# Kernel optimization log

Measured on AMD Instinct MI355X. Metric: run time of the kernel, lower is better.

Reference implementation:

```python
import jax, jax.numpy as jnp
import numpy as np

NUM_LEVELS = 6
LEVEL_DIM = 4
BASE_RES = 4
HASHMAP_SIZE = 2 ** 19  # torch-ngp default log2_hashmap_size=19
N_SAMPLES = 300
PRIMES = (1, 2654435761, 805459861)
N_RAYS = 16384

# offsets of the 8 trilinear corners, [8,3]
_OFFS = jnp.array([[i, j, k] for i in (0, 1) for j in (0, 1) for k in (0, 1)], dtype=jnp.int32)


def _sample_points_along_ray(starts, ends):
    # starts/ends: [N,2]; lerp 300 points, append ray parameter t as z -> [N,300,3]
    t = jnp.linspace(0.0, 1.0, N_SAMPLES, dtype=starts.dtype)[None, :, None]  # [1,300,1]
    p2 = starts[:, None, :] * (1.0 - t) + ends[:, None, :] * t  # [N,300,2]
    z = jnp.broadcast_to(t, (starts.shape[0], N_SAMPLES, 1))
    return jnp.concatenate([p2, z], axis=-1)


def _grid_encode(points, embeddings):
    # points: [N,S,3] in [0,1]; embeddings: [L, T, D]. Returns [N,S,L*D].
    feats = []
    for l in range(NUM_LEVELS):
        R = BASE_RES * (2 ** l)  # 4,8,16,32,64,128
        pos = points * R
        p0 = jnp.floor(pos).astype(jnp.int32)
        w = pos - p0  # trilinear fractions, [N,S,3]
        corners = jnp.clip(p0[..., None, :] + _OFFS, 0, R)  # [N,S,8,3]
        cw = jnp.where(_OFFS.astype(bool), w[..., None, :], 1.0 - w[..., None, :]).prod(-1)  # [N,S,8]
        if (R + 1) ** 3 <= HASHMAP_SIZE:
            # dense level: row-major vertex index
            idx = corners[..., 0] + corners[..., 1] * (R + 1) + corners[..., 2] * (R + 1) ** 2
        else:
            # hashed level: xor of coord * prime, uint32 wraparound
            c = corners.astype(jnp.uint32)
            idx = ((c[..., 0] * jnp.uint32(PRIMES[0]))
                   ^ (c[..., 1] * jnp.uint32(PRIMES[1]))
                   ^ (c[..., 2] * jnp.uint32(PRIMES[2]))) % jnp.uint32(HASHMAP_SIZE)
            idx = idx.astype(jnp.int32)
        emb = embeddings[l][idx]  # [N,S,8,D] gather
        feats.append((cw[..., None] * emb).sum(-2))  # [N,S,D]
    return jnp.concatenate(feats, axis=-1)  # [N,S,24]


def setup_inputs() -> dict:
    key = jax.random.key(0)
    ks = jax.random.split(key, 12)
    x = jax.random.uniform(ks[0], (N_RAYS, 4), dtype=jnp.float32)
    indices_first = jax.random.randint(ks[1], (N_RAYS,), 0, N_SAMPLES, dtype=jnp.int32)
    # hash-grid tables, torch-ngp init: uniform(-1e-4, 1e-4)
    embeddings = jax.random.uniform(ks[2], (NUM_LEVELS, HASHMAP_SIZE, LEVEL_DIM),
                                    minval=-1e-4, maxval=1e-4, dtype=jnp.float32)
    d_in = NUM_LEVELS * LEVEL_DIM * 5  # 120
    sc = 0.02
    W1 = jax.random.normal(ks[3], (64, d_in), dtype=jnp.float32) * sc
    b1 = jnp.zeros((64,), jnp.float32)
    W2 = jax.random.normal(ks[4], (64, 64), dtype=jnp.float32) * sc
    b2 = jnp.zeros((64,), jnp.float32)
    W3 = jax.random.normal(ks[5], (64, 64), dtype=jnp.float32) * sc
    b3 = jnp.zeros((64,), jnp.float32)
    W4 = jax.random.normal(ks[6], (3, 64), dtype=jnp.float32) * sc
    b4 = jnp.zeros((3,), jnp.float32)
    return {"x": x, "indices_first": indices_first, "embeddings": embeddings,
            "W1": W1, "b1": b1, "W2": W2, "b2": b2, "W3": W3, "b3": b3, "W4": W4, "b4": b4}


def reference(x, indices_first, embeddings, W1, b1, W2, b2, W3, b3, W4, b4):
    pts = jax.lax.stop_gradient(_sample_points_along_ray(x[:, :2], x[:, 2:4]))  # no_grad in original
    pe = _grid_encode(pts, embeddings)  # [N,300,24]
    n = jnp.arange(x.shape[0])
    gather = lambda d: pe[n, jnp.clip(indices_first + d, 0, N_SAMPLES - 1)]
    feat = jnp.concatenate([gather(-2), gather(-1), gather(0), gather(1), gather(2)], axis=-1)  # [N,120]
    h = jax.nn.relu(feat @ W1.T + b1)
    h = jax.nn.relu(h @ W2.T + b2)
    h = jax.nn.relu(h @ W3.T + b3)
    return h @ W4.T + b4  # [N,3]
```

## Files before the change

### kernel.cpp

```cpp
#include <hip/hip_runtime.h>


#define NSAMP 300
#define HSIZE (1u << 19)

__global__ __launch_bounds__(256, 6) void encode_kernel(
    const float4* __restrict__ x,
    const int*    __restrict__ idxf,
    const float4* __restrict__ emb,
    float4*       __restrict__ feat,
    int N)
{
    const int tid = threadIdx.x;
    const int r   = tid & 63;
    const int p   = blockIdx.y * 4 + (tid >> 6);
    const int ray = blockIdx.x * 64 + r;
    if (p >= 30) return;

    const float4 xr = x[ray];
    const int    i0 = idxf[ray];
    const int d = p / 6;
    const int l = p - d * 6;
    int s = i0 + d - 2;
    s = max(0, min(s, NSAMP - 1));
    const float t   = (float)s * (1.0f / 299.0f);
    const float omt = 1.0f - t;
    const int   R   = 4 << l;
    const float fR  = (float)R;
    const float px = (xr.x * omt + xr.z * t) * fR;
    const float py = (xr.y * omt + xr.w * t) * fR;
    const float pz = t * fR;
    const float fx0 = floorf(px), fy0 = floorf(py), fz0 = floorf(pz);
    const float wx = px - fx0, wy = py - fy0, wz = pz - fz0;
    const int ix = (int)fx0, iy = (int)fy0, iz = (int)fz0;
    const int Rp1 = R + 1;
    const float4* __restrict__ ebase = emb + (size_t)l * HSIZE;

    float ax = 0.f, ay = 0.f, az = 0.f, aw = 0.f;
    #pragma unroll
    for (int c = 0; c < 8; ++c) {
        const int ox = (c >> 2) & 1, oy = (c >> 1) & 1, oz = c & 1;
        int cx = min(ix + ox, R); cx = max(cx, 0);
        int cy = min(iy + oy, R); cy = max(cy, 0);
        int cz = min(iz + oz, R); cz = max(cz, 0);
        unsigned idx;
        if (l < 5) {
            idx = (unsigned)(cx + cy * Rp1 + cz * Rp1 * Rp1);
        } else {
            idx = ((unsigned)cx * 1u
                 ^ (unsigned)cy * 2654435761u
                 ^ (unsigned)cz * 805459861u) & (HSIZE - 1u);
        }
        const float4 e = ebase[idx];
        const float cw = (ox ? wx : 1.f - wx)
                       * (oy ? wy : 1.f - wy)
                       * (oz ? wz : 1.f - wz);
        ax = fmaf(cw, e.x, ax);
        ay = fmaf(cw, e.y, ay);
        az = fmaf(cw, e.z, az);
        aw = fmaf(cw, e.w, aw);
    }
    feat[(size_t)p * N + ray] = make_float4(ax, ay, az, aw);
}

__global__ __launch_bounds__(1024, 4) void mlp_kernel(
    const float4* __restrict__ feat,
    const float* __restrict__ W1, const float* __restrict__ b1,
    const float* __restrict__ W2, const float* __restrict__ b2,
    const float* __restrict__ W3, const float* __restrict__ b3,
    const float* __restrict__ W4, const float* __restrict__ b4,
    float* __restrict__ out, int N)
{
    __shared__ float sm[12288];
    float* sFeat = sm;
    float* sHa   = sm + 7936;
    float* sHb   = sm;

    const int tid = threadIdx.x;
    const int r   = tid & 63;
    const int w   = tid >> 6;
    const int ray = blockIdx.x * 64 + r;

    {
        const float4 v = feat[(size_t)w * N + ray];
        *(float4*)&sFeat[r * 124 + w * 4] = v;
        if (w < 14) {
            const float4 v2 = feat[(size_t)(w + 16) * N + ray];
            *(float4*)&sFeat[r * 124 + (w + 16) * 4] = v2;
        }
    }
    __syncthreads();

    const int j0 = w * 4;
    float hh[4];

    #pragma unroll
    for (int jj = 0; jj < 4; ++jj) hh[jj] = b1[j0 + jj];
    #pragma unroll 2
    for (int kc = 0; kc < 120; kc += 4) {
        const float4 f = *(const float4*)&sFeat[r * 124 + kc];
        #pragma unroll
        for (int jj = 0; jj < 4; ++jj) {
            const float4 wv = *(const float4*)&W1[(j0 + jj) * 120 + kc];
            hh[jj] = fmaf(f.x, wv.x, hh[jj]);
            hh[jj] = fmaf(f.y, wv.y, hh[jj]);
            hh[jj] = fmaf(f.z, wv.z, hh[jj]);
            hh[jj] = fmaf(f.w, wv.w, hh[jj]);
        }
    }
    {
        float4 o;
        o.x = fmaxf(hh[0], 0.f); o.y = fmaxf(hh[1], 0.f);
        o.z = fmaxf(hh[2], 0.f); o.w = fmaxf(hh[3], 0.f);
        *(float4*)&sHa[r * 68 + j0] = o;
    }
    __syncthreads();

    #pragma unroll
    for (int jj = 0; jj < 4; ++jj) hh[jj] = b2[j0 + jj];
    #pragma unroll 2
    for (int kc = 0; kc < 64; kc += 4) {
        const float4 f = *(const float4*)&sHa[r * 68 + kc];
        #pragma unroll
        for (int jj = 0; jj < 4; ++jj) {
            const float4 wv = *(const float4*)&W2[(j0 + jj) * 64 + kc];
            hh[jj] = fmaf(f.x, wv.x, hh[jj]);
            hh[jj] = fmaf(f.y, wv.y, hh[jj]);
            hh[jj] = fmaf(f.z, wv.z, hh[jj]);
            hh[jj] = fmaf(f.w, wv.w, hh[jj]);
        }
    }
    __syncthreads();
    {
        float4 o;
        o.x = fmaxf(hh[0], 0.f); o.y = fmaxf(hh[1], 0.f);
        o.z = fmaxf(hh[2], 0.f); o.w = fmaxf(hh[3], 0.f);
        *(float4*)&sHb[r * 68 + j0] = o;
    }
    __syncthreads();

    #pragma unroll
    for (int jj = 0; jj < 4; ++jj) hh[jj] = b3[j0 + jj];
    #pragma unroll 2
    for (int kc = 0; kc < 64; kc += 4) {
        const float4 f = *(const float4*)&sHb[r * 68 + kc];
        #pragma unroll
        for (int jj = 0; jj < 4; ++jj) {
            const float4 wv = *(const float4*)&W3[(j0 + jj) * 64 + kc];
            hh[jj] = fmaf(f.x, wv.x, hh[jj]);
            hh[jj] = fmaf(f.y, wv.y, hh[jj]);
            hh[jj] = fmaf(f.z, wv.z, hh[jj]);
            hh[jj] = fmaf(f.w, wv.w, hh[jj]);
        }
    }
    __syncthreads();
    {
        float4 o;
        o.x = fmaxf(hh[0], 0.f); o.y = fmaxf(hh[1], 0.f);
        o.z = fmaxf(hh[2], 0.f); o.w = fmaxf(hh[3], 0.f);
        *(float4*)&sHa[r * 68 + j0] = o;
    }
    __syncthreads();

    if (w < 3) {
        float acc = b4[w];
        #pragma unroll 2
        for (int kc = 0; kc < 64; kc += 4) {
            const float4 f  = *(const float4*)&sHa[r * 68 + kc];
            const float4 wv = *(const float4*)&W4[w * 64 + kc];
            acc = fmaf(f.x, wv.x, acc);
            acc = fmaf(f.y, wv.y, acc);
            acc = fmaf(f.z, wv.z, acc);
            acc = fmaf(f.w, wv.w, acc);
        }
        out[(size_t)ray * 3 + w] = acc;
    }
}

extern "C" void kernel_launch(void* const* d_in, const int* in_sizes, int n_in,
                              void* d_out, int out_size, void* d_ws, size_t ws_size,
                              hipStream_t stream) {
    const float4* x    = (const float4*)d_in[0];
    const int*    idxf = (const int*)   d_in[1];
    const float4* emb  = (const float4*)d_in[2];
    const float*  W1   = (const float*) d_in[3];
    const float*  b1   = (const float*) d_in[4];
    const float*  W2   = (const float*) d_in[5];
    const float*  b2   = (const float*) d_in[6];
    const float*  W3   = (const float*) d_in[7];
    const float*  b3   = (const float*) d_in[8];
    const float*  W4   = (const float*) d_in[9];
    const float*  b4   = (const float*) d_in[10];
    float* out = (float*)d_out;

    const int N = in_sizes[0] / 4;
    float4* feat = (float4*)d_ws;

    const int rayblocks = (N + 63) / 64;
    hipLaunchKernelGGL(encode_kernel, dim3(rayblocks, 8), dim3(256), 0, stream,
                       x, idxf, emb, feat, N);
    hipLaunchKernelGGL(mlp_kernel, dim3(rayblocks), dim3(1024), 0, stream,
                       feat, W1, b1, W2, b2, W3, b3, W4, b4, out, N);
}
```

Baseline: 146.2 us.

## Fuse hash-grid encoding and MLP into one kernel with 32-ray blocks

Merges the encode and MLP kernels into a single kernel. Each 512-thread block handles 32 rays and writes the encoded features straight into shared memory, so the global feature workspace round trip and the second launch go away. It also drops two barriers the MLP did not need and loads biases as float4. In exchange, each thread now computes up to two encodings in a loop, and the gather latency is overlapped only through occupancy within the fused block.

```diff
diff --git a/kernel.cpp b/kernel.cpp
--- a/kernel.cpp
+++ b/kernel.cpp
@@ -3,102 +3,94 @@
 
 #define NSAMP 300
 #define HSIZE (1u << 19)
+#define RAYS 32
+#define FSTRIDE 124
+#define HSTRIDE 68
 
-__global__ __launch_bounds__(256, 6) void encode_kernel(
+__global__ __launch_bounds__(512, 4) void rgbnet_fused(
     const float4* __restrict__ x,
     const int*    __restrict__ idxf,
     const float4* __restrict__ emb,
-    float4*       __restrict__ feat,
-    int N)
-{
-    const int tid = threadIdx.x;
-    const int r   = tid & 63;
-    const int p   = blockIdx.y * 4 + (tid >> 6);
-    const int ray = blockIdx.x * 64 + r;
-    if (p >= 30) return;
-
-    const float4 xr = x[ray];
-    const int    i0 = idxf[ray];
-    const int d = p / 6;
-    const int l = p - d * 6;
-    int s = i0 + d - 2;
-    s = max(0, min(s, NSAMP - 1));
-    const float t   = (float)s * (1.0f / 299.0f);
-    const float omt = 1.0f - t;
-    const int   R   = 4 << l;
-    const float fR  = (float)R;
-    const float px = (xr.x * omt + xr.z * t) * fR;
-    const float py = (xr.y * omt + xr.w * t) * fR;
-    const float pz = t * fR;
-    const float fx0 = floorf(px), fy0 = floorf(py), fz0 = floorf(pz);
-    const float wx = px - fx0, wy = py - fy0, wz = pz - fz0;
-    const int ix = (int)fx0, iy = (int)fy0, iz = (int)fz0;
-    const int Rp1 = R + 1;
-    const float4* __restrict__ ebase = emb + (size_t)l * HSIZE;
-
-    float ax = 0.f, ay = 0.f, az = 0.f, aw = 0.f;
-    #pragma unroll
-    for (int c = 0; c < 8; ++c) {
-        const int ox = (c >> 2) & 1, oy = (c >> 1) & 1, oz = c & 1;
-        int cx = min(ix + ox, R); cx = max(cx, 0);
-        int cy = min(iy + oy, R); cy = max(cy, 0);
-        int cz = min(iz + oz, R); cz = max(cz, 0);
-        unsigned idx;
-        if (l < 5) {
-            idx = (unsigned)(cx + cy * Rp1 + cz * Rp1 * Rp1);
-        } else {
-            idx = ((unsigned)cx * 1u
-                 ^ (unsigned)cy * 2654435761u
-                 ^ (unsigned)cz * 805459861u) & (HSIZE - 1u);
-        }
-        const float4 e = ebase[idx];
-        const float cw = (ox ? wx : 1.f - wx)
-                       * (oy ? wy : 1.f - wy)
-                       * (oz ? wz : 1.f - wz);
-        ax = fmaf(cw, e.x, ax);
-        ay = fmaf(cw, e.y, ay);
-        az = fmaf(cw, e.z, az);
-        aw = fmaf(cw, e.w, aw);
-    }
-    feat[(size_t)p * N + ray] = make_float4(ax, ay, az, aw);
-}
-
-__global__ __launch_bounds__(1024, 4) void mlp_kernel(
-    const float4* __restrict__ feat,
     const float* __restrict__ W1, const float* __restrict__ b1,
     const float* __restrict__ W2, const float* __restrict__ b2,
     const float* __restrict__ W3, const float* __restrict__ b3,
     const float* __restrict__ W4, const float* __restrict__ b4,
     float* __restrict__ out, int N)
 {
-    __shared__ float sm[12288];
+    __shared__ float sm[RAYS * FSTRIDE + RAYS * HSTRIDE];
     float* sFeat = sm;
-    float* sHa   = sm + 7936;
+    float* sHa   = sm + RAYS * FSTRIDE;
     float* sHb   = sm;
 
-    const int tid = threadIdx.x;
-    const int r   = tid & 63;
-    const int w   = tid >> 6;
-    const int ray = blockIdx.x * 64 + r;
+    const int tid  = threadIdx.x;
+    const int lane = tid & 63;
+    const int r    = lane & 31;
+    const int half = lane >> 5;
+    const int w    = tid >> 6;
+    const int u    = w * 2 + half;
+    const int ray  = blockIdx.x * RAYS + r;
 
     {
-        const float4 v = feat[(size_t)w * N + ray];
-        *(float4*)&sFeat[r * 124 + w * 4] = v;
-        if (w < 14) {
-            const float4 v2 = feat[(size_t)(w + 16) * N + ray];
-            *(float4*)&sFeat[r * 124 + (w + 16) * 4] = v2;
+        const float4 xr = x[ray];
+        const int    i0 = idxf[ray];
+
+        for (int p = u; p < 30; p += 16) {
+            const int d = p / 6;
+            const int l = p - d * 6;
+            int s = i0 + d - 2;
+            s = max(0, min(s, NSAMP - 1));
+            const float t   = (float)s * (1.0f / 299.0f);
+            const float omt = 1.0f - t;
+            const int   R   = 4 << l;
+            const float fR  = (float)R;
+            const float px = (xr.x * omt + xr.z * t) * fR;
+            const float py = (xr.y * omt + xr.w * t) * fR;
+            const float pz = t * fR;
+            const float fx0 = floorf(px), fy0 = floorf(py), fz0 = floorf(pz);
+            const float wx = px - fx0, wy = py - fy0, wz = pz - fz0;
+            const int ix = (int)fx0, iy = (int)fy0, iz = (int)fz0;
+            const int Rp1 = R + 1;
+            const float4* __restrict__ ebase = emb + (size_t)l * HSIZE;
+
+            float ax = 0.f, ay = 0.f, az = 0.f, aw = 0.f;
+            #pragma unroll
+            for (int c = 0; c < 8; ++c) {
+                const int ox = (c >> 2) & 1, oy = (c >> 1) & 1, oz = c & 1;
+                int cx = min(ix + ox, R); cx = max(cx, 0);
+                int cy = min(iy + oy, R); cy = max(cy, 0);
+                int cz = min(iz + oz, R); cz = max(cz, 0);
+                unsigned idx;
+                if (l < 5) {
+                    idx = (unsigned)(cx + cy * Rp1 + cz * Rp1 * Rp1);
+                } else {
+                    idx = ((unsigned)cx * 1u
+                         ^ (unsigned)cy * 2654435761u
+                         ^ (unsigned)cz * 805459861u) & (HSIZE - 1u);
+                }
+                const float4 e = ebase[idx];
+                const float cw = (ox ? wx : 1.f - wx)
+                               * (oy ? wy : 1.f - wy)
+                               * (oz ? wz : 1.f - wz);
+                ax = fmaf(cw, e.x, ax);
+                ay = fmaf(cw, e.y, ay);
+                az = fmaf(cw, e.z, az);
+                aw = fmaf(cw, e.w, aw);
+            }
+            *(float4*)&sFeat[r * FSTRIDE + p * 4] = make_float4(ax, ay, az, aw);
         }
     }
     __syncthreads();
 
-    const int j0 = w * 4;
+    const int j0 = u * 4;
     float hh[4];
 
-    #pragma unroll
-    for (int jj = 0; jj < 4; ++jj) hh[jj] = b1[j0 + jj];
+    {
+        const float4 bv = *(const float4*)&b1[j0];
+        hh[0] = bv.x; hh[1] = bv.y; hh[2] = bv.z; hh[3] = bv.w;
+    }
     #pragma unroll 2
     for (int kc = 0; kc < 120; kc += 4) {
-        const float4 f = *(const float4*)&sFeat[r * 124 + kc];
+        const float4 f = *(const float4*)&sFeat[r * FSTRIDE + kc];
         #pragma unroll
         for (int jj = 0; jj < 4; ++jj) {
             const float4 wv = *(const float4*)&W1[(j0 + jj) * 120 + kc];
@@ -112,15 +104,17 @@
         float4 o;
         o.x = fmaxf(hh[0], 0.f); o.y = fmaxf(hh[1], 0.f);
         o.z = fmaxf(hh[2], 0.f); o.w = fmaxf(hh[3], 0.f);
-        *(float4*)&sHa[r * 68 + j0] = o;
+        *(float4*)&sHa[r * HSTRIDE + j0] = o;
     }
     __syncthreads();
 
-    #pragma unroll
-    for (int jj = 0; jj < 4; ++jj) hh[jj] = b2[j0 + jj];
+    {
+        const float4 bv = *(const float4*)&b2[j0];
+        hh[0] = bv.x; hh[1] = bv.y; hh[2] = bv.z; hh[3] = bv.w;
+    }
     #pragma unroll 2
     for (int kc = 0; kc < 64; kc += 4) {
-        const float4 f = *(const float4*)&sHa[r * 68 + kc];
+        const float4 f = *(const float4*)&sHa[r * HSTRIDE + kc];
         #pragma unroll
         for (int jj = 0; jj < 4; ++jj) {
             const float4 wv = *(const float4*)&W2[(j0 + jj) * 64 + kc];
@@ -130,20 +124,21 @@
             hh[jj] = fmaf(f.w, wv.w, hh[jj]);
         }
     }
-    __syncthreads();
     {
         float4 o;
         o.x = fmaxf(hh[0], 0.f); o.y = fmaxf(hh[1], 0.f);
         o.z = fmaxf(hh[2], 0.f); o.w = fmaxf(hh[3], 0.f);
-        *(float4*)&sHb[r * 68 + j0] = o;
+        *(float4*)&sHb[r * HSTRIDE + j0] = o;
     }
     __syncthreads();
 
-    #pragma unroll
-    for (int jj = 0; jj < 4; ++jj) hh[jj] = b3[j0 + jj];
+    {
+        const float4 bv = *(const float4*)&b3[j0];
+        hh[0] = bv.x; hh[1] = bv.y; hh[2] = bv.z; hh[3] = bv.w;
+    }
     #pragma unroll 2
     for (int kc = 0; kc < 64; kc += 4) {
-        const float4 f = *(const float4*)&sHb[r * 68 + kc];
+        const float4 f = *(const float4*)&sHb[r * HSTRIDE + kc];
         #pragma unroll
         for (int jj = 0; jj < 4; ++jj) {
             const float4 wv = *(const float4*)&W3[(j0 + jj) * 64 + kc];
@@ -153,27 +148,26 @@
             hh[jj] = fmaf(f.w, wv.w, hh[jj]);
         }
     }
-    __syncthreads();
     {
         float4 o;
         o.x = fmaxf(hh[0], 0.f); o.y = fmaxf(hh[1], 0.f);
         o.z = fmaxf(hh[2], 0.f); o.w = fmaxf(hh[3], 0.f);
-        *(float4*)&sHa[r * 68 + j0] = o;
+        *(float4*)&sHa[r * HSTRIDE + j0] = o;
     }
     __syncthreads();
 
-    if (w < 3) {
-        float acc = b4[w];
+    if (u < 3) {
+        float acc = b4[u];
         #pragma unroll 2
         for (int kc = 0; kc < 64; kc += 4) {
-            const float4 f  = *(const float4*)&sHa[r * 68 + kc];
-            const float4 wv = *(const float4*)&W4[w * 64 + kc];
+            const float4 f  = *(const float4*)&sHa[r * HSTRIDE + kc];
+            const float4 wv = *(const float4*)&W4[u * 64 + kc];
             acc = fmaf(f.x, wv.x, acc);
             acc = fmaf(f.y, wv.y, acc);
             acc = fmaf(f.z, wv.z, acc);
             acc = fmaf(f.w, wv.w, acc);
         }
-        out[(size_t)ray * 3 + w] = acc;
+        out[(size_t)ray * 3 + u] = acc;
     }
 }
 
@@ -194,11 +188,7 @@
     float* out = (float*)d_out;
 
     const int N = in_sizes[0] / 4;
-    float4* feat = (float4*)d_ws;
-
-    const int rayblocks = (N + 63) / 64;
-    hipLaunchKernelGGL(encode_kernel, dim3(rayblocks, 8), dim3(256), 0, stream,
-                       x, idxf, emb, feat, N);
-    hipLaunchKernelGGL(mlp_kernel, dim3(rayblocks), dim3(1024), 0, stream,
-                       feat, W1, b1, W2, b2, W3, b3, W4, b4, out, N);
+    const int blocks = (N + RAYS - 1) / RAYS;
+    hipLaunchKernelGGL(rgbnet_fused, dim3(blocks), dim3(512), 0, stream,
+                       x, idxf, emb, W1, b1, W2, b2, W3, b3, W4, b4, out, N);
 }
```

Measured after the change: 140.4 us. -4.0%, faster.
